# Kernel tuning notes

Measured on AMD Instinct MI355X. Metric: run time of the kernel, lower is better.

Reference implementation:

```python
import jax, jax.numpy as jnp
import numpy as np

N_PER_G = 100  # nodes per graph


def setup_inputs() -> dict:
    key = jax.random.key(0)
    ks = jax.random.split(key, 12)
    N, G, E = 100000, 1000, 1600000
    ninp, nout, K, H, H2 = 3, 10, 5, 64, 32
    x = jax.random.normal(ks[0], (N, ninp), jnp.float32)
    # within-graph random edges (contiguous node blocks per graph)
    epg = E // G
    gid = jnp.arange(E, dtype=jnp.int32) // epg
    src = jax.random.randint(ks[1], (E,), 0, N_PER_G, jnp.int32) + gid * N_PER_G
    dst = jax.random.randint(ks[2], (E,), 0, N_PER_G, jnp.int32) + gid * N_PER_G
    edge_index = jnp.stack([src, dst])
    batch = (jnp.arange(N, dtype=jnp.int32) // N_PER_G)
    lambda_max = 1.5 + 0.5 * jax.random.uniform(ks[3], (G,), jnp.float32)
    s = 0.05
    W1 = jax.random.normal(ks[4], (K, ninp, H), jnp.float32) * s
    b1 = jnp.zeros((H,), jnp.float32)
    W2 = jax.random.normal(ks[5], (K, H, H), jnp.float32) * s
    b2 = jnp.zeros((H,), jnp.float32)
    W3 = jax.random.normal(ks[6], (K, H, H), jnp.float32) * s
    b3 = jnp.zeros((H,), jnp.float32)
    bn_gamma = jnp.ones((H,), jnp.float32)
    bn_beta = jnp.zeros((H,), jnp.float32)
    bn_mean = jnp.zeros((H,), jnp.float32)
    bn_var = jnp.ones((H,), jnp.float32)
    fc1_w = jax.random.normal(ks[7], (H, H2), jnp.float32) * s
    fc1_b = jnp.zeros((H2,), jnp.float32)
    fc2_w = jax.random.normal(ks[8], (H2, nout), jnp.float32) * s
    fc2_b = jnp.zeros((nout,), jnp.float32)
    return dict(x=x, edge_index=edge_index, batch=batch, lambda_max=lambda_max,
                W1=W1, b1=b1, W2=W2, b2=b2, W3=W3, b3=b3,
                bn_gamma=bn_gamma, bn_beta=bn_beta, bn_mean=bn_mean, bn_var=bn_var,
                fc1_w=fc1_w, fc1_b=fc1_b, fc2_w=fc2_w, fc2_b=fc2_b)


def _cheb_conv(x, W, b, row, col, coef_edge, coef_loop):
    # PyG ChebConv with sym-normalized scaled Laplacian:
    # Lhat x = scatter_add(coef_edge * x[col] -> row) + coef_loop * x
    N = x.shape[0]
    def lhat(h):
        return jax.ops.segment_sum(coef_edge[:, None] * h[col], row,
                                   num_segments=N) + coef_loop[:, None] * h
    Tx0 = x
    out = Tx0 @ W[0]
    Tx1 = lhat(x)
    out = out + Tx1 @ W[1]
    for k in range(2, W.shape[0]):
        Tx2 = 2.0 * lhat(Tx1) - Tx0
        out = out + Tx2 @ W[k]
        Tx0, Tx1 = Tx1, Tx2
    return out + b


def reference(x, edge_index, batch, lambda_max,
              W1, b1, W2, b2, W3, b3,
              bn_gamma, bn_beta, bn_mean, bn_var,
              fc1_w, fc1_b, fc2_w, fc2_b):
    N = x.shape[0]
    G = lambda_max.shape[0]
    row, col = edge_index[0], edge_index[1]
    # sym Laplacian normalization, scaled by 2/lambda_max (per-graph)
    deg = jax.ops.segment_sum(jnp.ones_like(row, dtype=x.dtype), row, num_segments=N)
    dis = jnp.where(deg > 0, deg, 1.0) ** -0.5
    dis = jnp.where(deg > 0, dis, 0.0)
    lmax_e = lambda_max[batch[row]]
    coef_edge = -(2.0 / lmax_e) * dis[row] * dis[col]   # off-diagonal of Lhat
    coef_loop = 2.0 / lambda_max[batch] - 1.0           # diagonal of Lhat
    h = jax.nn.relu(_cheb_conv(x, W1, b1, row, col, coef_edge, coef_loop))
    h = jax.nn.relu(_cheb_conv(h, W2, b2, row, col, coef_edge, coef_loop))
    h = jax.nn.relu(_cheb_conv(h, W3, b3, row, col, coef_edge, coef_loop))
    # global mean pool over graphs
    sums = jax.ops.segment_sum(h, batch, num_segments=G)
    cnts = jax.ops.segment_sum(jnp.ones((N,), h.dtype), batch, num_segments=G)
    g = sums / jnp.maximum(cnts, 1.0)[:, None]
    # BatchNorm1d (eval mode, running stats), eps=1e-5
    g = (g - bn_mean) * jax.lax.rsqrt(bn_var + 1e-5) * bn_gamma + bn_beta
    g = jax.nn.relu(g @ fc1_w + fc1_b)
    return jax.nn.log_softmax(g @ fc2_w + fc2_b, axis=1)
```

## Files before the change

### kernel.cpp

```cpp
#include <hip/hip_runtime.h>

#define NPG 100
#define HF 64
#define NROW 128
#define SA 120
#define ST 72
#define SAT 136

typedef float  f4   __attribute__((ext_vector_type(4)));
typedef float  f16v __attribute__((ext_vector_type(16)));
typedef short  bf8  __attribute__((ext_vector_type(8)));

#define SZ_ARM (NROW * SA * 2)
#define SZ_TRM (NROW * ST * 2)
#define SZ_TT  (HF * SAT * 2)
#define OFF_ARM 0
#define OFF_TRM SZ_ARM
#define OFF_TT  (OFF_TRM + SZ_TRM)
#define OFF_AF  OFF_TRM
#define OFF_MISC 70720
#define SMEM_BYTES (OFF_MISC + 1792)

#define WT_TOTAL 46080

__device__ __forceinline__ unsigned short f2bf(float f) {
    unsigned u = __float_as_uint(f);
    u += 0x7fffu + ((u >> 16) & 1u);
    return (unsigned short)(u >> 16);
}
__device__ __forceinline__ float bf2f(unsigned short h) {
    return __uint_as_float(((unsigned)h) << 16);
}
__device__ __forceinline__ f16v zerov16() {
    f16v z;
    #pragma unroll
    for (int i = 0; i < 16; i++) z[i] = 0.f;
    return z;
}

__global__ void wconv(const float* __restrict__ W1, const float* __restrict__ W2,
                      const float* __restrict__ W3, unsigned short* __restrict__ ws)
{
    int idx = blockIdx.x * 256 + threadIdx.x;
    if (idx >= WT_TOTAL) return;
    float v;
    if (idx < 5120) {
        int k5 = idx >> 10, rem = idx & 1023, fo = rem >> 4, fi = rem & 15;
        v = (fi < 3) ? W1[(k5 * 3 + fi) * HF + fo] : 0.f;
    } else if (idx < 25600) {
        int j = idx - 5120;
        int k5 = j >> 12, rem = j & 4095, fo = rem >> 6, fi = rem & 63;
        v = W2[(k5 * HF + fi) * HF + fo];
    } else {
        int j = idx - 25600;
        int k5 = j >> 12, rem = j & 4095, fo = rem >> 6, fi = rem & 63;
        v = W3[(k5 * HF + fi) * HF + fo];
    }
    ws[idx] = f2bf(v);
}

__launch_bounds__(256, 2)
__global__ void cheb32t(const float* __restrict__ x, const int* __restrict__ ei,
                        const float* __restrict__ lambda_max,
                        const unsigned short* __restrict__ Wt,
                        const float* __restrict__ b1, const float* __restrict__ b2,
                        const float* __restrict__ b3,
                        const float* __restrict__ bng, const float* __restrict__ bnb,
                        const float* __restrict__ bnm, const float* __restrict__ bnv,
                        const float* __restrict__ fc1w, const float* __restrict__ fc1b,
                        const float* __restrict__ fc2w, const float* __restrict__ fc2b,
                        float* __restrict__ out, int E_total, int epg)
{
    extern __shared__ char sm[];
    const int tid = threadIdx.x;
    const int g = blockIdx.x;
    const int ebase = g * epg, nbase = g * NPG;
    const int wg = tid >> 6, lane = tid & 63;
    const int l31 = lane & 31, hh = lane >> 5;
    const int ht  = wg & 1;
    const int Mt0 = (wg >> 1) * 2;
    const int fo  = ht * 32 + l31;

    float* Af     = (float*)(sm + OFF_AF);
    int*   deg    = (int*)(sm + OFF_MISC);
    float* dis    = (float*)(sm + OFF_MISC + 512);
    float* pool   = (float*)(sm + OFF_MISC + 1024);
    float* gvn    = (float*)(sm + OFF_MISC + 1280);
    float* zf     = (float*)(sm + OFF_MISC + 1536);
    float* logits = (float*)(sm + OFF_MISC + 1664);
    float* lsep   = (float*)(sm + OFF_MISC + 1728);

    const float lam = lambda_max[g];
    const float two_l = 2.0f / lam;
    const float cl = two_l - 1.0f;

    for (int i = tid; i < 2500; i += 256) ((f4*)Af)[i] = (f4){0.f, 0.f, 0.f, 0.f};
    if (tid < NPG) deg[tid] = 0;
    if (tid < HF) pool[tid] = 0.f;
    __syncthreads();
    for (int e = tid; e < epg; e += 256)
        atomicAdd(&deg[ei[ebase + e] - nbase], 1);
    __syncthreads();
    if (tid < NPG) dis[tid] = deg[tid] > 0 ? rsqrtf((float)deg[tid]) : 0.f;
    __syncthreads();
    for (int e = tid; e < epg; e += 256) {
        int r = ei[ebase + e] - nbase;
        int c = ei[E_total + ebase + e] - nbase;
        atomicAdd(&Af[r * NPG + c], -two_l * dis[r] * dis[c]);
    }
    __syncthreads();
    if (tid < NPG) Af[tid * NPG + tid] += cl;
    __syncthreads();
    for (int u = tid; u < NROW * 56; u += 256) {
        int n = u / 56, p = (u % 56) * 2;
        float v0 = (n < NPG && p     < NPG) ? Af[n * NPG + p]     : 0.f;
        float v1 = (n < NPG && p + 1 < NPG) ? Af[n * NPG + p + 1] : 0.f;
        *(unsigned*)(sm + OFF_ARM + (n * SA + p) * 2) =
            (unsigned)f2bf(v0) | ((unsigned)f2bf(v1) << 16);
    }
    __syncthreads();

    for (int i = tid; i < (SZ_TRM + SZ_TT) / 16; i += 256)
        ((f4*)(sm + OFF_TRM))[i] = (f4){0.f, 0.f, 0.f, 0.f};
    __syncthreads();
    if (tid < NPG) {
        unsigned short h0 = f2bf(x[(nbase + tid) * 3 + 0]);
        unsigned short h1 = f2bf(x[(nbase + tid) * 3 + 1]);
        unsigned short h2 = f2bf(x[(nbase + tid) * 3 + 2]);
        *(unsigned*)(sm + OFF_TRM + (tid * ST) * 2) = (unsigned)h0 | ((unsigned)h1 << 16);
        *(unsigned short*)(sm + OFF_TRM + (tid * ST + 2) * 2) = h2;
        *(unsigned short*)(sm + OFF_TT + (0 * SAT + tid) * 2) = h0;
        *(unsigned short*)(sm + OFF_TT + (1 * SAT + tid) * 2) = h1;
        *(unsigned short*)(sm + OFF_TT + (2 * SAT + tid) * 2) = h2;
    }
    __syncthreads();

    f16v acc[2];
    unsigned prev[2][8], oldr[2][8];
    const float* bsv[3] = {b1, b2, b3};

    for (int L = 0; L < 3; L++) {
        const bool l1 = (L == 0);
        const unsigned short* Wl = l1 ? Wt : (Wt + (L == 1 ? 5120 : 25600));
        acc[0] = zerov16();
        acc[1] = zerov16();

        #pragma unroll
        for (int m = 0; m < 2; m++) {
            int np = (Mt0 + m) * 32 + l31;
            #pragma unroll
            for (int q4 = 0; q4 < 4; q4++) {
                int fb = 8 * q4 + 4 * hh + 32 * ht;
                uint2 u = *(const uint2*)(sm + OFF_TRM + (np * ST + fb) * 2);
                prev[m][2 * q4] = u.x;
                prev[m][2 * q4 + 1] = u.y;
            }
        }

        auto TW = [&](int k5) {
            const int nKs = l1 ? 1 : 4;
            for (int Ks = 0; Ks < nKs; Ks++) {
                bf8 bw;
                if (l1) bw = *(const bf8*)(Wl + (k5 * 64 + fo) * 16 + 8 * hh);
                else    bw = *(const bf8*)(Wl + (k5 * 64 + fo) * 64 + Ks * 16 + 8 * hh);
                #pragma unroll
                for (int m = 0; m < 2; m++) {
                    bf8 a = *(const bf8*)(sm + OFF_TRM +
                              (((Mt0 + m) * 32 + l31) * ST + Ks * 16 + 8 * hh) * 2);
                    acc[m] = __builtin_amdgcn_mfma_f32_32x32x16_bf16(a, bw, acc[m], 0, 0, 0);
                }
            }
        };

        TW(0);
        for (int s = 1; s <= 4; s++) {
            bf8 af[7];
            #pragma unroll
            for (int Ks = 0; Ks < 7; Ks++)
                af[Ks] = *(const bf8*)(sm + OFF_TT +
                           ((32 * ht + l31) * SAT + Ks * 16 + 8 * hh) * 2);
            __syncthreads();
            #pragma unroll
            for (int m = 0; m < 2; m++) {
                int np = (Mt0 + m) * 32 + l31;
                f16v c = zerov16();
                #pragma unroll
                for (int Ks = 0; Ks < 7; Ks++) {
                    bf8 b = *(const bf8*)(sm + OFF_ARM + (np * SA + Ks * 16 + 8 * hh) * 2);
                    c = __builtin_amdgcn_mfma_f32_32x32x16_bf16(af[Ks], b, c, 0, 0, 0);
                }
                unsigned short h[16];
                #pragma unroll
                for (int r = 0; r < 16; r++) {
                    float v = c[r];
                    if (s >= 2) {
                        unsigned short o = (unsigned short)
                            ((oldr[m][r >> 1] >> (16 * (r & 1))) & 0xffff);
                        v = 2.f * v - bf2f(o);
                    }
                    h[r] = f2bf(v);
                }
                #pragma unroll
                for (int p = 0; p < 8; p++) {
                    oldr[m][p] = prev[m][p];
                    prev[m][p] = (unsigned)h[2 * p] | ((unsigned)h[2 * p + 1] << 16);
                }
                #pragma unroll
                for (int r = 0; r < 16; r++) {
                    int f = (r & 3) + 8 * (r >> 2) + 4 * hh + 32 * ht;
                    *(unsigned short*)(sm + OFF_TT + (f * SAT + np) * 2) = h[r];
                }
                #pragma unroll
                for (int q4 = 0; q4 < 4; q4++) {
                    int fb = 8 * q4 + 4 * hh + 32 * ht;
                    uint2 pk;
                    pk.x = prev[m][2 * q4];
                    pk.y = prev[m][2 * q4 + 1];
                    *(uint2*)(sm + OFF_TRM + (np * ST + fb) * 2) = pk;
                }
            }
            __syncthreads();
            TW(s);
        }
        __syncthreads();

        const float bias = bsv[L][fo];
        if (L < 2) {
            #pragma unroll
            for (int m = 0; m < 2; m++) {
                unsigned short h[16];
                #pragma unroll
                for (int r = 0; r < 16; r++) {
                    h[r] = f2bf(fmaxf(acc[m][r] + bias, 0.f));
                    int n = (Mt0 + m) * 32 + (r & 3) + 8 * (r >> 2) + 4 * hh;
                    *(unsigned short*)(sm + OFF_TRM + (n * ST + fo) * 2) = h[r];
                }
                #pragma unroll
                for (int q4 = 0; q4 < 4; q4++) {
                    int nb = (Mt0 + m) * 32 + 8 * q4 + 4 * hh;
                    uint2 pk;
                    pk.x = (unsigned)h[4 * q4] | ((unsigned)h[4 * q4 + 1] << 16);
                    pk.y = (unsigned)h[4 * q4 + 2] | ((unsigned)h[4 * q4 + 3] << 16);
                    *(uint2*)(sm + OFF_TT + (fo * SAT + nb) * 2) = pk;
                }
            }
            __syncthreads();
        } else {
            float ssum = 0.f;
            #pragma unroll
            for (int m = 0; m < 2; m++) {
                #pragma unroll
                for (int r = 0; r < 16; r++) {
                    int n = (Mt0 + m) * 32 + (r & 3) + 8 * (r >> 2) + 4 * hh;
                    float h = fmaxf(acc[m][r] + bias, 0.f);
                    if (n < NPG) ssum += h;
                }
            }
            ssum += __shfl_xor(ssum, 32, 64);
            if (hh == 0) atomicAdd(&pool[fo], ssum);
            __syncthreads();
        }
    }

    if (tid < HF) {
        float gv = pool[tid] * (1.0f / NPG);
        gv = (gv - bnm[tid]) * rsqrtf(bnv[tid] + 1e-5f) * bng[tid] + bnb[tid];
        gvn[tid] = gv;
    }
    __syncthreads();
    if (tid < 32) {
        float a = fc1b[tid];
        for (int f = 0; f < HF; f++) a += gvn[f] * fc1w[f * 32 + tid];
        zf[tid] = fmaxf(a, 0.f);
    }
    __syncthreads();
    if (tid < 10) {
        float a = fc2b[tid];
        for (int k = 0; k < 32; k++) a += zf[k] * fc2w[k * 10 + tid];
        logits[tid] = a;
    }
    __syncthreads();
    if (tid == 0) {
        float m = logits[0];
        for (int i = 1; i < 10; i++) m = fmaxf(m, logits[i]);
        float s = 0.f;
        for (int i = 0; i < 10; i++) s += expf(logits[i] - m);
        lsep[0] = m + logf(s);
    }
    __syncthreads();
    if (tid < 10) out[g * 10 + tid] = logits[tid] - lsep[0];
}

extern "C" void kernel_launch(void* const* d_in, const int* in_sizes, int n_in,
                              void* d_out, int out_size, void* d_ws, size_t ws_size,
                              hipStream_t stream) {
    const float* x    = (const float*)d_in[0];
    const int*   ei   = (const int*)d_in[1];
    const float* lmax = (const float*)d_in[3];
    const float* W1   = (const float*)d_in[4];
    const float* b1   = (const float*)d_in[5];
    const float* W2   = (const float*)d_in[6];
    const float* b2   = (const float*)d_in[7];
    const float* W3   = (const float*)d_in[8];
    const float* b3   = (const float*)d_in[9];
    const float* bng  = (const float*)d_in[10];
    const float* bnb  = (const float*)d_in[11];
    const float* bnm  = (const float*)d_in[12];
    const float* bnv  = (const float*)d_in[13];
    const float* fc1w = (const float*)d_in[14];
    const float* fc1b = (const float*)d_in[15];
    const float* fc2w = (const float*)d_in[16];
    const float* fc2b = (const float*)d_in[17];

    const int E = in_sizes[1] / 2;
    const int G = in_sizes[3];
    const int epg = E / G;

    unsigned short* Wt = (unsigned short*)d_ws;

    wconv<<<(WT_TOTAL + 255) / 256, 256, 0, stream>>>(W1, W2, W3, Wt);

    hipFuncSetAttribute((const void*)cheb32t,
                        hipFuncAttributeMaxDynamicSharedMemorySize, SMEM_BYTES);

    cheb32t<<<G, 256, SMEM_BYTES, stream>>>(x, ei, lmax, Wt, b1, b2, b3,
                                            bng, bnb, bnm, bnv, fc1w, fc1b, fc2w, fc2b,
                                            (float*)d_out, E, epg);
}
```

Before: 183.0 us.

## Build Laplacian from packed byte edge counts and drop transposed T buffer

Edge multiplicities are now counted into a packed 8-bit-per-entry count matrix with integer atomics, replacing the separate degree pass and the float atomic scatter into a dense fp32 adjacency. Degrees come from summing the packed counts. The transposed copy of the Chebyshev state is removed; the MFMA operands are swapped so the B fragment is gathered with strided scalar LDS reads from the single row-major buffer. The smaller LDS footprint allows raising launch bounds to three blocks per CU. The cost is many 2-byte strided LDS loads per step, and counts silently overflow if any node pair has more than 255 parallel edges.

```diff
diff --git a/kernel.cpp b/kernel.cpp
--- a/kernel.cpp
+++ b/kernel.cpp
@@ -5,21 +5,19 @@
 #define NROW 128
 #define SA 120
 #define ST 72
-#define SAT 136
+#define CMW 28
 
 typedef float  f4   __attribute__((ext_vector_type(4)));
 typedef float  f16v __attribute__((ext_vector_type(16)));
 typedef short  bf8  __attribute__((ext_vector_type(8)));
 
 #define SZ_ARM (NROW * SA * 2)
-#define SZ_TRM (NROW * ST * 2)
-#define SZ_TT  (HF * SAT * 2)
+#define SZ_T   (NROW * ST * 2)
 #define OFF_ARM 0
-#define OFF_TRM SZ_ARM
-#define OFF_TT  (OFF_TRM + SZ_TRM)
-#define OFF_AF  OFF_TRM
-#define OFF_MISC 70720
-#define SMEM_BYTES (OFF_MISC + 1792)
+#define OFF_T   SZ_ARM
+#define OFF_CM  SZ_ARM
+#define OFF_MISC (OFF_T + SZ_T)
+#define SMEM_BYTES (OFF_MISC + 1280)
 
 #define WT_TOTAL 46080
 
@@ -59,17 +57,17 @@
     ws[idx] = f2bf(v);
 }
 
-__launch_bounds__(256, 2)
-__global__ void cheb32t(const float* __restrict__ x, const int* __restrict__ ei,
-                        const float* __restrict__ lambda_max,
-                        const unsigned short* __restrict__ Wt,
-                        const float* __restrict__ b1, const float* __restrict__ b2,
-                        const float* __restrict__ b3,
-                        const float* __restrict__ bng, const float* __restrict__ bnb,
-                        const float* __restrict__ bnm, const float* __restrict__ bnv,
-                        const float* __restrict__ fc1w, const float* __restrict__ fc1b,
-                        const float* __restrict__ fc2w, const float* __restrict__ fc2b,
-                        float* __restrict__ out, int E_total, int epg)
+__launch_bounds__(256, 3)
+__global__ void cheb1b(const float* __restrict__ x, const int* __restrict__ ei,
+                       const float* __restrict__ lambda_max,
+                       const unsigned short* __restrict__ Wt,
+                       const float* __restrict__ b1, const float* __restrict__ b2,
+                       const float* __restrict__ b3,
+                       const float* __restrict__ bng, const float* __restrict__ bnb,
+                       const float* __restrict__ bnm, const float* __restrict__ bnv,
+                       const float* __restrict__ fc1w, const float* __restrict__ fc1b,
+                       const float* __restrict__ fc2w, const float* __restrict__ fc2b,
+                       float* __restrict__ out, int E_total, int epg)
 {
     extern __shared__ char sm[];
     const int tid = threadIdx.x;
@@ -81,57 +79,66 @@
     const int Mt0 = (wg >> 1) * 2;
     const int fo  = ht * 32 + l31;
 
-    float* Af     = (float*)(sm + OFF_AF);
-    int*   deg    = (int*)(sm + OFF_MISC);
-    float* dis    = (float*)(sm + OFF_MISC + 512);
-    float* pool   = (float*)(sm + OFF_MISC + 1024);
-    float* gvn    = (float*)(sm + OFF_MISC + 1280);
-    float* zf     = (float*)(sm + OFF_MISC + 1536);
-    float* logits = (float*)(sm + OFF_MISC + 1664);
-    float* lsep   = (float*)(sm + OFF_MISC + 1728);
+    unsigned* Cm  = (unsigned*)(sm + OFF_CM);
+    float* dis    = (float*)(sm + OFF_MISC);
+    float* pool   = (float*)(sm + OFF_MISC + 448);
+    float* gvn    = (float*)(sm + OFF_MISC + 704);
+    float* zf     = (float*)(sm + OFF_MISC + 960);
+    float* logits = (float*)(sm + OFF_MISC + 1088);
+    float* lsep   = (float*)(sm + OFF_MISC + 1152);
 
     const float lam = lambda_max[g];
     const float two_l = 2.0f / lam;
     const float cl = two_l - 1.0f;
 
-    for (int i = tid; i < 2500; i += 256) ((f4*)Af)[i] = (f4){0.f, 0.f, 0.f, 0.f};
-    if (tid < NPG) deg[tid] = 0;
-    if (tid < HF) pool[tid] = 0.f;
-    __syncthreads();
-    for (int e = tid; e < epg; e += 256)
-        atomicAdd(&deg[ei[ebase + e] - nbase], 1);
-    __syncthreads();
-    if (tid < NPG) dis[tid] = deg[tid] > 0 ? rsqrtf((float)deg[tid]) : 0.f;
+    for (int i = tid; i < (NROW * CMW) / 4; i += 256)
+        ((f4*)Cm)[i] = (f4){0.f, 0.f, 0.f, 0.f};
     __syncthreads();
     for (int e = tid; e < epg; e += 256) {
         int r = ei[ebase + e] - nbase;
         int c = ei[E_total + ebase + e] - nbase;
-        atomicAdd(&Af[r * NPG + c], -two_l * dis[r] * dis[c]);
-    }
-    __syncthreads();
-    if (tid < NPG) Af[tid * NPG + tid] += cl;
+        atomicAdd(&Cm[r * CMW + (c >> 2)], 1u << (8 * (c & 3)));
+    }
+    __syncthreads();
+    if (tid < NPG) {
+        unsigned s = 0;
+        #pragma unroll
+        for (int w = 0; w < CMW; w++) {
+            unsigned u = Cm[tid * CMW + w];
+            s += (u & 255) + ((u >> 8) & 255) + ((u >> 16) & 255) + (u >> 24);
+        }
+        dis[tid] = s > 0 ? rsqrtf((float)s) : 0.f;
+    }
     __syncthreads();
     for (int u = tid; u < NROW * 56; u += 256) {
         int n = u / 56, p = (u % 56) * 2;
-        float v0 = (n < NPG && p     < NPG) ? Af[n * NPG + p]     : 0.f;
-        float v1 = (n < NPG && p + 1 < NPG) ? Af[n * NPG + p + 1] : 0.f;
+        float v0 = 0.f, v1 = 0.f;
+        if (n < NPG) {
+            unsigned w = Cm[n * CMW + (p >> 2)];
+            int sh = 8 * (p & 3);
+            float c0 = (float)((w >> sh) & 255);
+            float c1 = (float)((w >> (sh + 8)) & 255);
+            float base = -two_l * dis[n];
+            v0 = (p     < NPG) ? c0 * base * dis[p]     : 0.f;
+            v1 = (p + 1 < NPG) ? c1 * base * dis[p + 1] : 0.f;
+            if (p == n)     v0 += cl;
+            if (p + 1 == n) v1 += cl;
+        }
         *(unsigned*)(sm + OFF_ARM + (n * SA + p) * 2) =
             (unsigned)f2bf(v0) | ((unsigned)f2bf(v1) << 16);
     }
     __syncthreads();
 
-    for (int i = tid; i < (SZ_TRM + SZ_TT) / 16; i += 256)
-        ((f4*)(sm + OFF_TRM))[i] = (f4){0.f, 0.f, 0.f, 0.f};
+    for (int i = tid; i < SZ_T / 16; i += 256)
+        ((f4*)(sm + OFF_T))[i] = (f4){0.f, 0.f, 0.f, 0.f};
+    if (tid < HF) pool[tid] = 0.f;
     __syncthreads();
     if (tid < NPG) {
         unsigned short h0 = f2bf(x[(nbase + tid) * 3 + 0]);
         unsigned short h1 = f2bf(x[(nbase + tid) * 3 + 1]);
         unsigned short h2 = f2bf(x[(nbase + tid) * 3 + 2]);
-        *(unsigned*)(sm + OFF_TRM + (tid * ST) * 2) = (unsigned)h0 | ((unsigned)h1 << 16);
-        *(unsigned short*)(sm + OFF_TRM + (tid * ST + 2) * 2) = h2;
-        *(unsigned short*)(sm + OFF_TT + (0 * SAT + tid) * 2) = h0;
-        *(unsigned short*)(sm + OFF_TT + (1 * SAT + tid) * 2) = h1;
-        *(unsigned short*)(sm + OFF_TT + (2 * SAT + tid) * 2) = h2;
+        *(unsigned*)(sm + OFF_T + (tid * ST) * 2) = (unsigned)h0 | ((unsigned)h1 << 16);
+        *(unsigned short*)(sm + OFF_T + (tid * ST + 2) * 2) = h2;
     }
     __syncthreads();
 
@@ -147,14 +154,15 @@
 
         #pragma unroll
         for (int m = 0; m < 2; m++) {
-            int np = (Mt0 + m) * 32 + l31;
-            #pragma unroll
-            for (int q4 = 0; q4 < 4; q4++) {
-                int fb = 8 * q4 + 4 * hh + 32 * ht;
-                uint2 u = *(const uint2*)(sm + OFF_TRM + (np * ST + fb) * 2);
-                prev[m][2 * q4] = u.x;
-                prev[m][2 * q4 + 1] = u.y;
-            }
+            unsigned short tv[16];
+            #pragma unroll
+            for (int r = 0; r < 16; r++) {
+                int np = (Mt0 + m) * 32 + (r & 3) + 8 * (r >> 2) + 4 * hh;
+                tv[r] = *(const unsigned short*)(sm + OFF_T + (np * ST + fo) * 2);
+            }
+            #pragma unroll
+            for (int p = 0; p < 8; p++)
+                prev[m][p] = (unsigned)tv[2 * p] | ((unsigned)tv[2 * p + 1] << 16);
         }
 
         auto TW = [&](int k5) {
@@ -165,7 +173,7 @@
                 else    bw = *(const bf8*)(Wl + (k5 * 64 + fo) * 64 + Ks * 16 + 8 * hh);
                 #pragma unroll
                 for (int m = 0; m < 2; m++) {
-                    bf8 a = *(const bf8*)(sm + OFF_TRM +
+                    bf8 a = *(const bf8*)(sm + OFF_T +
                               (((Mt0 + m) * 32 + l31) * ST + Ks * 16 + 8 * hh) * 2);
                     acc[m] = __builtin_amdgcn_mfma_f32_32x32x16_bf16(a, bw, acc[m], 0, 0, 0);
                 }
@@ -174,20 +182,24 @@
 
         TW(0);
         for (int s = 1; s <= 4; s++) {
-            bf8 af[7];
-            #pragma unroll
-            for (int Ks = 0; Ks < 7; Ks++)
-                af[Ks] = *(const bf8*)(sm + OFF_TT +
-                           ((32 * ht + l31) * SAT + Ks * 16 + 8 * hh) * 2);
+            bf8 bfr[7];
+            #pragma unroll
+            for (int Ks = 0; Ks < 7; Ks++) {
+                #pragma unroll
+                for (int j = 0; j < 8; j++) {
+                    int k = Ks * 16 + 8 * hh + j;
+                    bfr[Ks][j] = *(const short*)(sm + OFF_T + (k * ST + fo) * 2);
+                }
+            }
             __syncthreads();
             #pragma unroll
             for (int m = 0; m < 2; m++) {
-                int np = (Mt0 + m) * 32 + l31;
                 f16v c = zerov16();
                 #pragma unroll
                 for (int Ks = 0; Ks < 7; Ks++) {
-                    bf8 b = *(const bf8*)(sm + OFF_ARM + (np * SA + Ks * 16 + 8 * hh) * 2);
-                    c = __builtin_amdgcn_mfma_f32_32x32x16_bf16(af[Ks], b, c, 0, 0, 0);
+                    bf8 a = *(const bf8*)(sm + OFF_ARM +
+                              (((Mt0 + m) * 32 + l31) * SA + Ks * 16 + 8 * hh) * 2);
+                    c = __builtin_amdgcn_mfma_f32_32x32x16_bf16(a, bfr[Ks], c, 0, 0, 0);
                 }
                 unsigned short h[16];
                 #pragma unroll
@@ -207,16 +219,8 @@
                 }
                 #pragma unroll
                 for (int r = 0; r < 16; r++) {
-                    int f = (r & 3) + 8 * (r >> 2) + 4 * hh + 32 * ht;
-                    *(unsigned short*)(sm + OFF_TT + (f * SAT + np) * 2) = h[r];
-                }
-                #pragma unroll
-                for (int q4 = 0; q4 < 4; q4++) {
-                    int fb = 8 * q4 + 4 * hh + 32 * ht;
-                    uint2 pk;
-                    pk.x = prev[m][2 * q4];
-                    pk.y = prev[m][2 * q4 + 1];
-                    *(uint2*)(sm + OFF_TRM + (np * ST + fb) * 2) = pk;
+                    int np = (Mt0 + m) * 32 + (r & 3) + 8 * (r >> 2) + 4 * hh;
+                    *(unsigned short*)(sm + OFF_T + (np * ST + fo) * 2) = h[r];
                 }
             }
             __syncthreads();
@@ -228,20 +232,11 @@
         if (L < 2) {
             #pragma unroll
             for (int m = 0; m < 2; m++) {
-                unsigned short h[16];
                 #pragma unroll
                 for (int r = 0; r < 16; r++) {
-                    h[r] = f2bf(fmaxf(acc[m][r] + bias, 0.f));
-                    int n = (Mt0 + m) * 32 + (r & 3) + 8 * (r >> 2) + 4 * hh;
-                    *(unsigned short*)(sm + OFF_TRM + (n * ST + fo) * 2) = h[r];
-                }
-                #pragma unroll
-                for (int q4 = 0; q4 < 4; q4++) {
-                    int nb = (Mt0 + m) * 32 + 8 * q4 + 4 * hh;
-                    uint2 pk;
-                    pk.x = (unsigned)h[4 * q4] | ((unsigned)h[4 * q4 + 1] << 16);
-                    pk.y = (unsigned)h[4 * q4 + 2] | ((unsigned)h[4 * q4 + 3] << 16);
-                    *(uint2*)(sm + OFF_TT + (fo * SAT + nb) * 2) = pk;
+                    float h = fmaxf(acc[m][r] + bias, 0.f);
+                    int np = (Mt0 + m) * 32 + (r & 3) + 8 * (r >> 2) + 4 * hh;
+                    *(unsigned short*)(sm + OFF_T + (np * ST + fo) * 2) = f2bf(h);
                 }
             }
             __syncthreads();
@@ -251,9 +246,9 @@
             for (int m = 0; m < 2; m++) {
                 #pragma unroll
                 for (int r = 0; r < 16; r++) {
-                    int n = (Mt0 + m) * 32 + (r & 3) + 8 * (r >> 2) + 4 * hh;
+                    int np = (Mt0 + m) * 32 + (r & 3) + 8 * (r >> 2) + 4 * hh;
                     float h = fmaxf(acc[m][r] + bias, 0.f);
-                    if (n < NPG) ssum += h;
+                    if (np < NPG) ssum += h;
                 }
             }
             ssum += __shfl_xor(ssum, 32, 64);
@@ -320,10 +315,10 @@
 
     wconv<<<(WT_TOTAL + 255) / 256, 256, 0, stream>>>(W1, W2, W3, Wt);
 
-    hipFuncSetAttribute((const void*)cheb32t,
+    hipFuncSetAttribute((const void*)cheb1b,
                         hipFuncAttributeMaxDynamicSharedMemorySize, SMEM_BYTES);
 
-    cheb32t<<<G, 256, SMEM_BYTES, stream>>>(x, ei, lmax, Wt, b1, b2, b3,
-                                            bng, bnb, bnm, bnv, fc1w, fc1b, fc2w, fc2b,
-                                            (float*)d_out, E, epg);
-}
+    cheb1b<<<G, 256, SMEM_BYTES, stream>>>(x, ei, lmax, Wt, b1, b2, b3,
+                                           bng, bnb, bnm, bnv, fc1w, fc1b, fc2w, fc2b,
+                                           (float*)d_out, E, epg);
+}
```

Result: slower. 360.8 us (+97.1%).
